# Kernel tuning notes

Measured on AMD Instinct MI355X. Metric: run time of the kernel, lower is better.

The kernel has to match this reference:

```python
import jax, jax.numpy as jnp
import numpy as np

BN_EPS = 1e-5
L2_EPS = 1e-12


def setup_inputs() -> dict:
    key = jax.random.key(0)
    ks = jax.random.split(key, 4)
    B, C, H, W = 16, 384, 56, 56
    x = jax.random.normal(ks[0], (B, C, H, W), dtype=jnp.float32)
    w_qkv = jax.random.normal(ks[1], (3 * C, C), dtype=jnp.float32) * (1.0 / np.sqrt(C))
    b_qkv = jnp.zeros((3 * C,), dtype=jnp.float32)
    w_proj = jax.random.normal(ks[2], (C, C), dtype=jnp.float32) * (1.0 / np.sqrt(C))
    b_proj = jnp.zeros((C,), dtype=jnp.float32)
    bn_gamma = jnp.ones((C,), dtype=jnp.float32)
    bn_beta = jnp.zeros((C,), dtype=jnp.float32)
    bn_mean = jnp.zeros((C,), dtype=jnp.float32)
    bn_var = jnp.ones((C,), dtype=jnp.float32)
    temperature = jnp.ones((1,), dtype=jnp.float32)
    return {"x": x, "w_qkv": w_qkv, "b_qkv": b_qkv, "w_proj": w_proj,
            "b_proj": b_proj, "bn_gamma": bn_gamma, "bn_beta": bn_beta,
            "bn_mean": bn_mean, "bn_var": bn_var, "temperature": temperature}


def _l2norm_lastdim(t):
    # F.normalize(t, dim=-1): divide by max(||t||_2, eps)
    n = jnp.sqrt(jnp.sum(t * t, axis=-1, keepdims=True))
    return t / jnp.maximum(n, L2_EPS)


def reference(x, w_qkv, b_qkv, w_proj, b_proj, bn_gamma, bn_beta, bn_mean, bn_var, temperature):
    B, C, H, W = x.shape
    N = H * W
    # BatchNorm2d (eval mode, running stats)
    scale = bn_gamma / jnp.sqrt(bn_var + BN_EPS)          # [C]
    shift = bn_beta - bn_mean * scale                     # [C]
    xn = x * scale[None, :, None, None] + shift[None, :, None, None]
    # 1x1 conv qkv: C -> 3C, operate on flattened spatial [B, C, N]
    xn_f = xn.reshape(B, C, N)
    qkv = jnp.einsum('oc,bcn->bon', w_qkv, xn_f) + b_qkv[None, :, None]  # [B,3C,N]
    q, k, v = qkv[:, :C], qkv[:, C:2 * C], qkv[:, 2 * C:]
    q = _l2norm_lastdim(q)                                # [B,C,N]
    k = _l2norm_lastdim(k)
    # channel-transposed attention: [B,C,C]
    logits = jnp.einsum('bcn,bdn->bcd', q, k) * temperature[0]
    attn = jax.nn.softmax(logits, axis=-1)
    fused = jnp.einsum('bcd,bdn->bcn', attn, v)           # [B,C,N]
    # 1x1 proj conv + residual
    out = jnp.einsum('oc,bcn->bon', w_proj, fused) + b_proj[None, :, None]
    return x + out.reshape(B, C, H, W)
```

## Files before the change

### kernel.cpp

```cpp
#include <hip/hip_runtime.h>

#define BATCH 16
#define CCH   384
#define NSP   3136
#define NSPP  3200
#define OQKV  1152
#define KSPL  5

typedef unsigned short u16;
typedef float  f32x4  __attribute__((ext_vector_type(4)));
typedef __bf16 bf16x8 __attribute__((ext_vector_type(8)));

__device__ __forceinline__ float bf2f(u16 u) {
  union { unsigned int i; float f; } v; v.i = ((unsigned int)u) << 16; return v.f;
}
__device__ __forceinline__ u16 f2bf(float f) {
  union { float f; unsigned int i; } v; v.f = f;
  unsigned int i = v.i;
  return (u16)((i + 0x7fffu + ((i >> 16) & 1u)) >> 16);
}
__device__ __forceinline__ float rdf(const void* p, long i, bool bf) {
  return bf ? bf2f(((const u16*)p)[i]) : ((const float*)p)[i];
}

__device__ __forceinline__ void gload_lds16(const u16* g, u16* l) {
  __builtin_amdgcn_global_load_lds(
      (const __attribute__((address_space(1))) void*)g,
      (__attribute__((address_space(3))) void*)l, 16, 0, 0);
}

__global__ void transpose_kernel(const void* __restrict__ x, u16* __restrict__ xt,
                                 const u16* __restrict__ probe) {
  const bool bf = (probe[0] == 0x3F80u);
  __shared__ float Ls[32 * 65];
  const int t = threadIdx.x;
  const int n0 = blockIdx.x * 64, c0 = blockIdx.y * 32, b = blockIdx.z;
  if (n0 >= NSP) {
    const int n_l = t >> 2, c8 = (t & 3) * 8;
    uint4 zq = make_uint4(0, 0, 0, 0);
    *(uint4*)(xt + ((long)b * NSPP + n0 + n_l) * CCH + c0 + c8) = zq;
    return;
  }
  {
    const int c_l = t >> 3, n8 = (t & 7) * 8;
    const long src = ((long)b * CCH + c0 + c_l) * NSP + n0 + n8;
    float v[8];
    if (bf) {
      union { uint4 q; u16 e[8]; } u; u.q = *(const uint4*)((const u16*)x + src);
      #pragma unroll
      for (int i = 0; i < 8; i++) v[i] = bf2f(u.e[i]);
    } else {
      float4 a = *(const float4*)((const float*)x + src);
      float4 c = *(const float4*)((const float*)x + src + 4);
      v[0]=a.x; v[1]=a.y; v[2]=a.z; v[3]=a.w; v[4]=c.x; v[5]=c.y; v[6]=c.z; v[7]=c.w;
    }
    #pragma unroll
    for (int i = 0; i < 8; i++) Ls[c_l * 65 + n8 + i] = v[i];
  }
  __syncthreads();
  {
    const int n_l = t >> 2, c8 = (t & 3) * 8;
    union { uint4 q; u16 e[8]; } o;
    #pragma unroll
    for (int i = 0; i < 8; i++) o.e[i] = f2bf(Ls[(c8 + i) * 65 + n_l]);
    *(uint4*)(xt + ((long)b * NSPP + n0 + n_l) * CCH + c0 + c8) = o.q;
  }
}

__global__ void prep_kernel(const void* __restrict__ w_qkv, const void* __restrict__ b_qkv,
                            const void* __restrict__ gamma, const void* __restrict__ beta,
                            const void* __restrict__ mean,  const void* __restrict__ var,
                            const void* __restrict__ b_proj, const void* __restrict__ w_proj,
                            u16* __restrict__ w_eff, float* __restrict__ b_eff,
                            float* __restrict__ bproj_f, u16* __restrict__ wp_bf,
                            const u16* __restrict__ probe) {
  const bool bf = (probe[0] == 0x3F80u);
  __shared__ float s_scale[CCH], s_shift[CCH];
  const int tid = threadIdx.x;
  for (int c = tid; c < CCH; c += 128) {
    float g = rdf(gamma, c, bf), bt = rdf(beta, c, bf);
    float mn = rdf(mean, c, bf), vr = rdf(var, c, bf);
    float sc = g * rsqrtf(vr + 1e-5f);
    s_scale[c] = sc; s_shift[c] = bt - mn * sc;
  }
  __syncthreads();
  const int o = blockIdx.x;
  float part = 0.f;
  for (int c = tid; c < CCH; c += 128) {
    float w = rdf(w_qkv, (long)o * CCH + c, bf);
    w_eff[o * CCH + c] = f2bf(w * s_scale[c]);
    part += w * s_shift[c];
  }
  for (int off = 32; off > 0; off >>= 1) part += __shfl_down(part, off, 64);
  __shared__ float s_part[2];
  if ((tid & 63) == 0) s_part[tid >> 6] = part;
  __syncthreads();
  if (tid == 0) b_eff[o] = rdf(b_qkv, o, bf) + s_part[0] + s_part[1];
  if (o < CCH) {
    for (int c = tid; c < CCH; c += 128)
      wp_bf[o * CCH + c] = f2bf(rdf(w_proj, (long)o * CCH + c, bf));
  }
  if (o == 0) {
    for (int c = tid; c < CCH; c += 128) bproj_f[c] = rdf(b_proj, c, bf);
  }
}

__global__ void zero_kernel(float4* __restrict__ p, long n4) {
  for (long i = (long)blockIdx.x * blockDim.x + threadIdx.x; i < n4;
       i += (long)gridDim.x * blockDim.x)
    p[i] = make_float4(0.f, 0.f, 0.f, 0.f);
}

template<int BM, int BN, int WGM, int WGN, int OUTM, bool BIASM, bool BIASN, bool RES,
         int KS, bool QKN, int NCHK>
__launch_bounds__(256)
__global__ void gemm_nt(const u16* __restrict__ A, const u16* __restrict__ B,
                        void* __restrict__ Cv,
                        const float* __restrict__ biasm, const float* __restrict__ biasn,
                        const void* __restrict__ resv,
                        int K, int lda, int ldb, int ldc,
                        long sA, long sB, long sC, long sRes, int zb, int nLim,
                        float* __restrict__ qns,
                        const u16* __restrict__ probe) {
  constexpr int WM = BM / WGM, WN = BN / WGN;
  constexpr int FM = WM / 16,  FN = WN / 16;
  constexpr int NA = BM / 32,  NB = BN / 32;
  const bool f32io = (probe[0] != 0x3F80u);
  __shared__ __align__(16) u16 As[BM * 64];
  __shared__ __align__(16) u16 Bs[BN * 64];
  const int tid = threadIdx.x, wave = tid >> 6, lane = tid & 63;
  const int quad = lane >> 4, l16 = lane & 15;
  const int wm = wave / WGN, wn = wave % WGN;
  int z = blockIdx.z, kc = 0;
  if (KS > 1) { kc = z % KS; z /= KS; }
  A += z * sA; B += z * sB;
  const long cOff = (long)(zb + z) * sC;
  const long rOff = (long)(zb + z) * sRes;

  const int gx = gridDim.x;
  const int tot = gx * gridDim.y;
  const int wg = blockIdx.y * gx + blockIdx.x;
  const int qq = tot >> 3, rr = tot & 7;
  const int xcd = wg & 7, idx = wg >> 3;
  const int nid = (xcd < rr ? xcd * (qq + 1) : rr * (qq + 1) + (xcd - rr) * qq) + idx;
  const int m0 = (nid % gx) * BM, n0 = (nid / gx) * BN;

  const int kLen = K / KS, kBeg = kc * kLen;

  const u16* ag[NA];
  const u16* bg[NB];
  #pragma unroll
  for (int p = 0; p < NA; p++) {
    int u = tid + p * 256, r = u >> 3, k8 = u & 7;
    ag[p] = A + (long)(m0 + r) * lda + kBeg + ((k8 ^ (r & 7)) << 3);
  }
  #pragma unroll
  for (int p = 0; p < NB; p++) {
    int u = tid + p * 256, r = u >> 3, k8 = u & 7;
    bg[p] = B + (long)(n0 + r) * ldb + kBeg + ((k8 ^ (r & 7)) << 3);
  }

  f32x4 acc[FM][FN] = {};

  const int nt = kLen >> 6;
  for (int t = 0; t < nt; t++) {
    #pragma unroll
    for (int p = 0; p < NA; p++) { gload_lds16(ag[p], &As[(p * 256 + wave * 64) * 8]); ag[p] += 64; }
    #pragma unroll
    for (int p = 0; p < NB; p++) { gload_lds16(bg[p], &Bs[(p * 256 + wave * 64) * 8]); bg[p] += 64; }
    __syncthreads();

    #pragma unroll
    for (int tt = 0; tt < 2; tt++) {
      bf16x8 af[FM], bfr[FN];
      #pragma unroll
      for (int f = 0; f < FM; f++) {
        int r = wm * WM + f * 16 + l16;
        af[f] = *(const bf16x8*)&As[r * 64 + (((tt * 4 + quad) ^ (l16 & 7)) << 3)];
      }
      #pragma unroll
      for (int g = 0; g < FN; g++) {
        int r = wn * WN + g * 16 + l16;
        bfr[g] = *(const bf16x8*)&Bs[r * 64 + (((tt * 4 + quad) ^ (l16 & 7)) << 3)];
      }
      #pragma unroll
      for (int f = 0; f < FM; f++)
        #pragma unroll
        for (int g = 0; g < FN; g++)
          acc[f][g] = __builtin_amdgcn_mfma_f32_16x16x32_bf16(af[f], bfr[g], acc[f][g], 0, 0, 0);
    }
    __syncthreads();
  }

  #pragma unroll
  for (int f = 0; f < FM; f++) {
    #pragma unroll
    for (int reg = 0; reg < 4; reg++) {
      const int mm = m0 + wm * WM + f * 16 + quad * 4 + reg;
      float s2 = 0.f;
      #pragma unroll
      for (int g = 0; g < FN; g++) {
        int nn = n0 + wn * WN + g * 16 + l16;
        float v = acc[f][g][reg];
        if (BIASM) v += biasm[mm];
        if (BIASN) v += biasn[nn];
        if (NCHK == 1 && nn >= nLim) v = 0.f;
        long off = (long)mm * ldc + nn;
        bool live = (NCHK != 2) || (nn < nLim);
        if (RES && live) {
          long ro = rOff + off;
          v += f32io ? ((const float*)resv)[ro] : bf2f(((const u16*)resv)[ro]);
        }
        if (OUTM == 1) {
          long po = cOff + off + ((KS > 1) ? (long)kc * sRes : 0L);
          ((float*)Cv)[po] = v;
        } else if (OUTM == 2) {
          if (live) {
            if (f32io) ((float*)Cv)[cOff + off] = v;
            else       ((u16*)Cv)[cOff + off]   = f2bf(v);
          }
        } else {
          ((u16*)Cv)[cOff + off] = f2bf(v);
        }
        if (QKN) s2 += v * v;
      }
      if (QKN) {
        s2 += __shfl_xor(s2, 1, 16);
        s2 += __shfl_xor(s2, 2, 16);
        s2 += __shfl_xor(s2, 4, 16);
        s2 += __shfl_xor(s2, 8, 16);
        if (l16 == 0) atomicAdd(qns + (long)(zb + z) * 768 + mm, s2);
      }
    }
  }
}

__global__ void softmax_kernel(const float* __restrict__ logits, const float* __restrict__ sums,
                               const void* __restrict__ temp, u16* __restrict__ attn,
                               int zb, const u16* __restrict__ probe) {
  const bool bfm = (probe[0] == 0x3F80u);
  const int c = blockIdx.x, b = blockIdx.y;
  const long base = ((long)b * KSPL) * (CCH * CCH) + (long)c * CCH;
  const float rq = 1.f / fmaxf(sqrtf(sums[(zb + b) * 768 + c]), 1e-12f);
  const float T = rdf(temp, 0, bfm);
  const int tid = threadIdx.x;
  float v[3]; float mx = -1e30f;
  #pragma unroll
  for (int j = 0; j < 3; j++) {
    int d = tid + j * 128;
    float lv = 0.f;
    #pragma unroll
    for (int kc = 0; kc < KSPL; kc++) lv += logits[base + (long)kc * CCH * CCH + d];
    float rd = 1.f / fmaxf(sqrtf(sums[(zb + b) * 768 + 384 + d]), 1e-12f);
    float xv = lv * rq * rd * T;
    v[j] = xv; mx = fmaxf(mx, xv);
  }
  for (int off = 32; off > 0; off >>= 1) mx = fmaxf(mx, __shfl_down(mx, off, 64));
  __shared__ float sm[2];
  if ((tid & 63) == 0) sm[tid >> 6] = mx;
  __syncthreads();
  mx = fmaxf(sm[0], sm[1]);
  float s = 0.f;
  #pragma unroll
  for (int j = 0; j < 3; j++) { v[j] = __expf(v[j] - mx); s += v[j]; }
  for (int off = 32; off > 0; off >>= 1) s += __shfl_down(s, off, 64);
  __shared__ float ss[2];
  if ((tid & 63) == 0) ss[tid >> 6] = s;
  __syncthreads();
  s = ss[0] + ss[1];
  const float inv = 1.f / s;
  u16* arow = attn + ((long)b * CCH + c) * CCH;
  #pragma unroll
  for (int j = 0; j < 3; j++) arow[tid + j * 128] = f2bf(v[j] * inv);
}

extern "C" void kernel_launch(void* const* d_in, const int* in_sizes, int n_in,
                              void* d_out, int out_size, void* d_ws, size_t ws_size,
                              hipStream_t stream) {
  const void* x      = d_in[0];
  const void* w_qkv  = d_in[1];
  const void* b_qkv  = d_in[2];
  const void* w_proj = d_in[3];
  const void* b_proj = d_in[4];
  const void* gamma  = d_in[5];
  const void* beta   = d_in[6];
  const void* mean   = d_in[7];
  const void* var    = d_in[8];
  const void* temp   = d_in[9];
  const u16* probe = (const u16*)gamma;

  const size_t SZ_XT    = (size_t)BATCH * NSPP * CCH * 2;
  const size_t SZ_WEFF  = (size_t)OQKV * CCH * 2;
  const size_t SZ_WPBF  = (size_t)CCH * CCH * 2;
  const size_t SZ_BEFF  = (size_t)OQKV * 4;
  const size_t SZ_BPROJ = (size_t)CCH * 4;
  const size_t SZ_SUMS  = (size_t)BATCH * 768 * 4;
  const size_t SZ_QK_B  = (size_t)768 * NSPP * 2;
  const size_t SZ_VT_B  = (size_t)NSPP * CCH * 2;
  const size_t SZ_FT_B  = (size_t)NSPP * CCH * 2;
  const size_t SZ_LOG_B = (size_t)KSPL * CCH * CCH * 4;
  const size_t SZ_ATT_B = (size_t)CCH * CCH * 2;
  const size_t P = SZ_QK_B + SZ_VT_B + SZ_FT_B + SZ_LOG_B + SZ_ATT_B;
  const size_t FIXED = SZ_XT + SZ_WEFF + SZ_WPBF + SZ_BEFF + SZ_BPROJ + SZ_SUMS;

  long chunk = 1;
  if (ws_size >= FIXED + P) {
    chunk = (long)((ws_size - FIXED) / P);
    if (chunk > BATCH) chunk = BATCH;
    if (chunk < 1) chunk = 1;
  }

  char* ws = (char*)d_ws;
  u16*   xt      = (u16*)ws;   ws += SZ_XT;
  u16*   w_eff   = (u16*)ws;   ws += SZ_WEFF;
  u16*   wp_bf   = (u16*)ws;   ws += SZ_WPBF;
  float* b_eff   = (float*)ws; ws += SZ_BEFF;
  float* bproj_f = (float*)ws; ws += SZ_BPROJ;
  float* sums    = (float*)ws; ws += SZ_SUMS;
  float* logits  = (float*)ws; ws += SZ_LOG_B * chunk;
  u16*   attn    = (u16*)ws;   ws += SZ_ATT_B * chunk;
  u16*   qk      = (u16*)ws;   ws += SZ_QK_B * chunk;
  u16*   v_t     = (u16*)ws;   ws += SZ_VT_B * chunk;
  u16*   fused_t = (u16*)ws;   ws += SZ_FT_B * chunk;

  transpose_kernel<<<dim3(NSPP / 64, CCH / 32, BATCH), dim3(256), 0, stream>>>(x, xt, probe);
  prep_kernel<<<dim3(OQKV), dim3(128), 0, stream>>>(
      w_qkv, b_qkv, gamma, beta, mean, var, b_proj, w_proj,
      w_eff, b_eff, bproj_f, wp_bf, probe);
  zero_kernel<<<dim3(12), dim3(256), 0, stream>>>((float4*)sums, (long)BATCH * 768 / 4);

  const long sX  = (long)CCH * NSP;
  const long sXT = (long)NSPP * CCH;
  const long sQK = (long)768 * NSPP;
  const long sVT = (long)NSPP * CCH;
  const long sFT = (long)NSPP * CCH;
  const long sLG = (long)KSPL * CCH * CCH;
  const long sAT = (long)CCH * CCH;

  for (long b0 = 0; b0 < BATCH; b0 += chunk) {
    const int nb = (int)((BATCH - b0) < chunk ? (BATCH - b0) : chunk);
    const u16* xtb = xt + b0 * sXT;

    gemm_nt<128, 128, 2, 2, 0, true, false, false, 1, true, 1>
        <<<dim3(6, 25, nb), dim3(256), 0, stream>>>(
        w_eff, xtb, qk, b_eff, nullptr, nullptr,
        CCH, CCH, CCH, NSPP, 0L, sXT, sQK, 0L, (int)b0, NSP, sums, probe);

    gemm_nt<128, 128, 2, 2, 0, false, true, false, 1, false, 0>
        <<<dim3(25, 3, nb), dim3(256), 0, stream>>>(
        xtb, w_eff + (long)768 * CCH, v_t, nullptr, b_eff + 768, nullptr,
        CCH, CCH, CCH, CCH, sXT, 0L, sVT, 0L, 0, 0, nullptr, probe);

    gemm_nt<128, 128, 2, 2, 1, false, false, false, KSPL, false, 0>
        <<<dim3(3, 3, nb * KSPL), dim3(256), 0, stream>>>(
        qk, qk + (long)CCH * NSPP, logits, nullptr, nullptr, nullptr,
        NSPP, NSPP, NSPP, CCH, sQK, sQK, sLG, (long)CCH * CCH, 0, 0, nullptr, probe);

    softmax_kernel<<<dim3(CCH, nb), dim3(128), 0, stream>>>(
        logits, sums, temp, attn, (int)b0, probe);

    gemm_nt<128, 128, 2, 2, 0, false, false, false, 1, false, 0>
        <<<dim3(25, 3, nb), dim3(256), 0, stream>>>(
        v_t, attn, fused_t, nullptr, nullptr, nullptr,
        CCH, CCH, CCH, CCH, sVT, sAT, sFT, 0L, 0, 0, nullptr, probe);

    gemm_nt<128, 128, 2, 2, 2, true, false, true, 1, false, 2>
        <<<dim3(3, 25, nb), dim3(256), 0, stream>>>(
        wp_bf, fused_t, d_out, bproj_f, nullptr, x,
        CCH, CCH, CCH, NSP, 0L, sFT, sX, sX, (int)b0, NSP, nullptr, probe);
  }
}
```

Before: 439.5 us.

## Double-buffer LDS tiles in gemm_nt to overlap global loads with MFMA

Splits the shared-memory A/B tiles into two buffers and restructures the K loop so the next tile's global_load_lds is issued while MFMAs run on the current one. Partial vmcnt waits and explicit barriers replace the full sync after each tile, so global-load latency is meant to be hidden behind compute. The cost is twice the LDS per block, which may lower occupancy. The hardcoded vmcnt(8) assumes exactly eight loads per stage (NA+NB==8), so any template instantiation with a different count could wait on the wrong loads.

```diff
diff --git a/kernel.cpp b/kernel.cpp
--- a/kernel.cpp
+++ b/kernel.cpp
@@ -10,6 +10,9 @@
 typedef unsigned short u16;
 typedef float  f32x4  __attribute__((ext_vector_type(4)));
 typedef __bf16 bf16x8 __attribute__((ext_vector_type(8)));
+
+#define WAITV(N) asm volatile("s_waitcnt vmcnt(%0)" :: "n"(N) : "memory")
+#define BARR do { __builtin_amdgcn_s_barrier(); __builtin_amdgcn_sched_barrier(0); } while (0)
 
 __device__ __forceinline__ float bf2f(u16 u) {
   union { unsigned int i; float f; } v; v.i = ((unsigned int)u) << 16; return v.f;
@@ -126,8 +129,10 @@
   constexpr int FM = WM / 16,  FN = WN / 16;
   constexpr int NA = BM / 32,  NB = BN / 32;
   const bool f32io = (probe[0] != 0x3F80u);
-  __shared__ __align__(16) u16 As[BM * 64];
-  __shared__ __align__(16) u16 Bs[BN * 64];
+  __shared__ __align__(16) u16 As0[BM * 64];
+  __shared__ __align__(16) u16 As1[BM * 64];
+  __shared__ __align__(16) u16 Bs0[BN * 64];
+  __shared__ __align__(16) u16 Bs1[BN * 64];
   const int tid = threadIdx.x, wave = tid >> 6, lane = tid & 63;
   const int quad = lane >> 4, l16 = lane & 15;
   const int wm = wave / WGN, wn = wave % WGN;
@@ -162,26 +167,25 @@
 
   f32x4 acc[FM][FN] = {};
 
-  const int nt = kLen >> 6;
-  for (int t = 0; t < nt; t++) {
-    #pragma unroll
-    for (int p = 0; p < NA; p++) { gload_lds16(ag[p], &As[(p * 256 + wave * 64) * 8]); ag[p] += 64; }
-    #pragma unroll
-    for (int p = 0; p < NB; p++) { gload_lds16(bg[p], &Bs[(p * 256 + wave * 64) * 8]); bg[p] += 64; }
-    __syncthreads();
-
+  auto stage = [&](u16* dA, u16* dB) {
+    #pragma unroll
+    for (int p = 0; p < NA; p++) { gload_lds16(ag[p], dA + (p * 256 + wave * 64) * 8); ag[p] += 64; }
+    #pragma unroll
+    for (int p = 0; p < NB; p++) { gload_lds16(bg[p], dB + (p * 256 + wave * 64) * 8); bg[p] += 64; }
+  };
+  auto compute = [&](const u16* sAp, const u16* sBp) {
     #pragma unroll
     for (int tt = 0; tt < 2; tt++) {
       bf16x8 af[FM], bfr[FN];
       #pragma unroll
       for (int f = 0; f < FM; f++) {
         int r = wm * WM + f * 16 + l16;
-        af[f] = *(const bf16x8*)&As[r * 64 + (((tt * 4 + quad) ^ (l16 & 7)) << 3)];
+        af[f] = *(const bf16x8*)&sAp[r * 64 + (((tt * 4 + quad) ^ (l16 & 7)) << 3)];
       }
       #pragma unroll
       for (int g = 0; g < FN; g++) {
         int r = wn * WN + g * 16 + l16;
-        bfr[g] = *(const bf16x8*)&Bs[r * 64 + (((tt * 4 + quad) ^ (l16 & 7)) << 3)];
+        bfr[g] = *(const bf16x8*)&sBp[r * 64 + (((tt * 4 + quad) ^ (l16 & 7)) << 3)];
       }
       #pragma unroll
       for (int f = 0; f < FM; f++)
@@ -189,7 +193,27 @@
         for (int g = 0; g < FN; g++)
           acc[f][g] = __builtin_amdgcn_mfma_f32_16x16x32_bf16(af[f], bfr[g], acc[f][g], 0, 0, 0);
     }
-    __syncthreads();
+  };
+
+  const int nt = kLen >> 6;
+  stage(As0, Bs0);
+  if (nt > 1) { stage(As1, Bs1); WAITV(8); }
+  else        { WAITV(0); }
+  BARR;
+  int t = 0;
+  while (true) {
+    compute(As0, Bs0);
+    if (++t == nt) break;
+    BARR;
+    if (t + 1 < nt) { stage(As0, Bs0); WAITV(8); }
+    else            { WAITV(0); }
+    BARR;
+    compute(As1, Bs1);
+    if (++t == nt) break;
+    BARR;
+    if (t + 1 < nt) { stage(As1, Bs1); WAITV(8); }
+    else            { WAITV(0); }
+    BARR;
   }
 
   #pragma unroll
```

New measurement: 468.3 us. +6.6%, slower.

## Reformulate attention via Gram matrix of input instead of materializing QKV

Applied to the files above, without the earlier changes.

The QKV projection over all spatial positions is replaced by a per-batch Gram matrix G = X·Xᵀ (symmetric, only lower blocks computed, split-K with a reduce kernel). Logits, the q/k norms and the bias corrections then come from small CxC products with the weights (Wq·G·Wkᵀ plus rank-one terms from row sums of X). The value and output projections are folded into one CxC matrix Wp·Wv·attn that is applied to X in a single final GEMM. This removes the large Q/K/V and fused intermediates and most of the spatial-dimension GEMM work, but adds many small kernels and uses hi/lo bf16 splitting to limit precision loss in the reassociated products.

```diff
diff --git a/kernel.cpp b/kernel.cpp
--- a/kernel.cpp
+++ b/kernel.cpp
@@ -4,8 +4,6 @@
 #define CCH   384
 #define NSP   3136
 #define NSPP  3200
-#define OQKV  1152
-#define KSPL  5
 
 typedef unsigned short u16;
 typedef float  f32x4  __attribute__((ext_vector_type(4)));
@@ -30,7 +28,7 @@
 }
 
 __global__ void transpose_kernel(const void* __restrict__ x, u16* __restrict__ xt,
-                                 const u16* __restrict__ probe) {
+                                 u16* __restrict__ xbf, const u16* __restrict__ probe) {
   const bool bf = (probe[0] == 0x3F80u);
   __shared__ float Ls[32 * 65];
   const int t = threadIdx.x;
@@ -54,8 +52,10 @@
       float4 c = *(const float4*)((const float*)x + src + 4);
       v[0]=a.x; v[1]=a.y; v[2]=a.z; v[3]=a.w; v[4]=c.x; v[5]=c.y; v[6]=c.z; v[7]=c.w;
     }
-    #pragma unroll
-    for (int i = 0; i < 8; i++) Ls[c_l * 65 + n8 + i] = v[i];
+    union { uint4 q; u16 e[8]; } ob;
+    #pragma unroll
+    for (int i = 0; i < 8; i++) { ob.e[i] = f2bf(v[i]); Ls[c_l * 65 + n8 + i] = v[i]; }
+    *(uint4*)(xbf + src) = ob.q;
   }
   __syncthreads();
   {
@@ -72,7 +72,9 @@
                             const void* __restrict__ mean,  const void* __restrict__ var,
                             const void* __restrict__ b_proj, const void* __restrict__ w_proj,
                             u16* __restrict__ w_eff, float* __restrict__ b_eff,
-                            float* __restrict__ bproj_f, u16* __restrict__ wp_bf,
+                            float* __restrict__ bproj_f,
+                            unsigned* __restrict__ w2qk, unsigned* __restrict__ wp2,
+                            u16* __restrict__ wvT,
                             const u16* __restrict__ probe) {
   const bool bf = (probe[0] == 0x3F80u);
   __shared__ float s_scale[CCH], s_shift[CCH];
@@ -88,7 +90,10 @@
   float part = 0.f;
   for (int c = tid; c < CCH; c += 128) {
     float w = rdf(w_qkv, (long)o * CCH + c, bf);
-    w_eff[o * CCH + c] = f2bf(w * s_scale[c]);
+    u16 wv = f2bf(w * s_scale[c]);
+    w_eff[(long)o * CCH + c] = wv;
+    if (o < 768) w2qk[(long)o * CCH + c] = (unsigned)wv | ((unsigned)wv << 16);
+    else         wvT[(long)c * CCH + (o - 768)] = wv;
     part += w * s_shift[c];
   }
   for (int off = 32; off > 0; off >>= 1) part += __shfl_down(part, off, 64);
@@ -97,8 +102,10 @@
   __syncthreads();
   if (tid == 0) b_eff[o] = rdf(b_qkv, o, bf) + s_part[0] + s_part[1];
   if (o < CCH) {
-    for (int c = tid; c < CCH; c += 128)
-      wp_bf[o * CCH + c] = f2bf(rdf(w_proj, (long)o * CCH + c, bf));
+    for (int c = tid; c < CCH; c += 128) {
+      u16 pv = f2bf(rdf(w_proj, (long)o * CCH + c, bf));
+      wp2[(long)o * CCH + c] = (unsigned)pv | ((unsigned)pv << 16);
+    }
   }
   if (o == 0) {
     for (int c = tid; c < CCH; c += 128) bproj_f[c] = rdf(b_proj, c, bf);
@@ -111,16 +118,18 @@
     p[i] = make_float4(0.f, 0.f, 0.f, 0.f);
 }
 
-template<int BM, int BN, int WGM, int WGN, int OUTM, bool BIASM, bool BIASN, bool RES,
-         int KS, bool QKN, int NCHK>
+template<int BM, int BN, int WGM, int WGN, int OUTM, bool BIASM, bool RES,
+         int NCHK, bool EPIL, bool SUMX, bool SYMM>
 __launch_bounds__(256)
 __global__ void gemm_nt(const u16* __restrict__ A, const u16* __restrict__ B,
                         void* __restrict__ Cv,
-                        const float* __restrict__ biasm, const float* __restrict__ biasn,
+                        const float* __restrict__ biasm,
                         const void* __restrict__ resv,
                         int K, int lda, int ldb, int ldc,
-                        long sA, long sB, long sC, long sRes, int zb, int nLim,
-                        float* __restrict__ qns,
+                        long sA, long sB, long sC, long sRes,
+                        int zb, int nLim, int ks, int sBM,
+                        float* __restrict__ qns, const u16* __restrict__ epW,
+                        float* __restrict__ sxp,
                         const u16* __restrict__ probe) {
   constexpr int WM = BM / WGM, WN = BN / WGN;
   constexpr int FM = WM / 16,  FN = WN / 16;
@@ -132,7 +141,7 @@
   const int quad = lane >> 4, l16 = lane & 15;
   const int wm = wave / WGN, wn = wave % WGN;
   int z = blockIdx.z, kc = 0;
-  if (KS > 1) { kc = z % KS; z /= KS; }
+  if (ks > 1) { kc = z % ks; z /= ks; }
   A += z * sA; B += z * sB;
   const long cOff = (long)(zb + z) * sC;
   const long rOff = (long)(zb + z) * sRes;
@@ -144,8 +153,9 @@
   const int xcd = wg & 7, idx = wg >> 3;
   const int nid = (xcd < rr ? xcd * (qq + 1) : rr * (qq + 1) + (xcd - rr) * qq) + idx;
   const int m0 = (nid % gx) * BM, n0 = (nid / gx) * BN;
-
-  const int kLen = K / KS, kBeg = kc * kLen;
+  if (SYMM && n0 > m0) return;
+
+  const int kLen = K / ks, kBeg = kc * kLen;
 
   const u16* ag[NA];
   const u16* bg[NB];
@@ -161,6 +171,7 @@
   }
 
   f32x4 acc[FM][FN] = {};
+  float rs[FM] = {};
 
   const int nt = kLen >> 6;
   for (int t = 0; t < nt; t++) {
@@ -182,6 +193,14 @@
       for (int g = 0; g < FN; g++) {
         int r = wn * WN + g * 16 + l16;
         bfr[g] = *(const bf16x8*)&Bs[r * 64 + (((tt * 4 + quad) ^ (l16 & 7)) << 3)];
+      }
+      if (SUMX) {
+        if (n0 == 0 && wn == 0) {
+          #pragma unroll
+          for (int f = 0; f < FM; f++)
+            #pragma unroll
+            for (int j = 0; j < 8; j++) rs[f] += (float)af[f][j];
+        }
       }
       #pragma unroll
       for (int f = 0; f < FM; f++)
@@ -192,6 +211,18 @@
     __syncthreads();
   }
 
+  if (SUMX) {
+    if (n0 == 0 && wn == 0) {
+      #pragma unroll
+      for (int f = 0; f < FM; f++) {
+        float r = rs[f];
+        r += __shfl_xor(r, 16, 64);
+        r += __shfl_xor(r, 32, 64);
+        if (quad == 0) atomicAdd(sxp + (long)z * CCH + m0 + wm * WM + f * 16 + l16, r);
+      }
+    }
+  }
+
   #pragma unroll
   for (int f = 0; f < FM; f++) {
     #pragma unroll
@@ -202,29 +233,34 @@
       for (int g = 0; g < FN; g++) {
         int nn = n0 + wn * WN + g * 16 + l16;
         float v = acc[f][g][reg];
-        if (BIASM) v += biasm[mm];
-        if (BIASN) v += biasn[nn];
-        if (NCHK == 1 && nn >= nLim) v = 0.f;
+        if (BIASM) v += biasm[(long)(zb + z) * sBM + mm];
         long off = (long)mm * ldc + nn;
-        bool live = (NCHK != 2) || (nn < nLim);
+        bool live = true;
+        if (NCHK == 2) live = (nn < nLim);
+        if (NCHK == 3) live = (mm < nLim);
         if (RES && live) {
           long ro = rOff + off;
           v += f32io ? ((const float*)resv)[ro] : bf2f(((const u16*)resv)[ro]);
         }
+        if (EPIL) s2 += v * bf2f(epW[(long)mm * CCH + nn]);
         if (OUTM == 1) {
-          long po = cOff + off + ((KS > 1) ? (long)kc * sRes : 0L);
-          ((float*)Cv)[po] = v;
+          ((float*)Cv)[cOff + off + (long)kc * sRes] = v;
         } else if (OUTM == 2) {
           if (live) {
             if (f32io) ((float*)Cv)[cOff + off] = v;
             else       ((u16*)Cv)[cOff + off]   = f2bf(v);
           }
+        } else if (OUTM == 4) {
+          if (live) {
+            u16 hi = f2bf(v);
+            u16 lo = f2bf(v - bf2f(hi));
+            ((unsigned*)Cv)[cOff + off] = (unsigned)hi | ((unsigned)lo << 16);
+          }
         } else {
-          ((u16*)Cv)[cOff + off] = f2bf(v);
+          if (live) ((u16*)Cv)[cOff + off] = f2bf(v);
         }
-        if (QKN) s2 += v * v;
-      }
-      if (QKN) {
+      }
+      if (EPIL) {
         s2 += __shfl_xor(s2, 1, 16);
         s2 += __shfl_xor(s2, 2, 16);
         s2 += __shfl_xor(s2, 4, 16);
@@ -235,25 +271,61 @@
   }
 }
 
-__global__ void softmax_kernel(const float* __restrict__ logits, const float* __restrict__ sums,
-                               const void* __restrict__ temp, u16* __restrict__ attn,
-                               int zb, const u16* __restrict__ probe) {
+__global__ void greduce_kernel(const float* __restrict__ Gp, unsigned* __restrict__ Gs,
+                               int kspl) {
+  const int b = blockIdx.y;
+  const int idx = blockIdx.x * 256 + threadIdx.x;
+  const int r = idx / CCH, c = idx % CCH;
+  const long e = ((r >> 7) >= (c >> 7)) ? ((long)r * CCH + c) : ((long)c * CCH + r);
+  const long base = (long)b * kspl * (CCH * CCH);
+  float s = 0.f;
+  for (int k = 0; k < kspl; k++) s += Gp[base + (long)k * (CCH * CCH) + e];
+  u16 hi = f2bf(s);
+  u16 lo = f2bf(s - bf2f(hi));
+  Gs[(long)b * (CCH * CCH) + idx] = (unsigned)hi | ((unsigned)lo << 16);
+}
+
+__global__ void ugemv_kernel(const u16* __restrict__ w_eff, const float* __restrict__ sx,
+                             float* __restrict__ u) {
+  const int m = blockIdx.x, b = blockIdx.y, l = threadIdx.x;
+  float s = 0.f;
+  for (int k = l; k < CCH; k += 64) s += bf2f(w_eff[(long)m * CCH + k]) * sx[b * CCH + k];
+  for (int off = 32; off > 0; off >>= 1) s += __shfl_down(s, off, 64);
+  if (l == 0) u[b * 768 + m] = s;
+}
+
+__global__ void cgemv_kernel(const unsigned* __restrict__ wp2, const float* __restrict__ av,
+                             const float* __restrict__ bproj, float* __restrict__ cvec) {
+  const int o = blockIdx.x, b = blockIdx.y, l = threadIdx.x;
+  float s = 0.f;
+  for (int c = l; c < CCH; c += 64)
+    s += bf2f((u16)(wp2[(long)o * CCH + c] & 0xffffu)) * av[b * CCH + c];
+  for (int off = 32; off > 0; off >>= 1) s += __shfl_down(s, off, 64);
+  if (l == 0) cvec[b * CCH + o] = s + bproj[o];
+}
+
+__global__ void softmax_kernel(const float* __restrict__ Lg, const float* __restrict__ qn2,
+                               const float* __restrict__ u, const float* __restrict__ beff,
+                               const void* __restrict__ temp,
+                               u16* __restrict__ attn, float* __restrict__ av,
+                               const u16* __restrict__ probe) {
   const bool bfm = (probe[0] == 0x3F80u);
-  const int c = blockIdx.x, b = blockIdx.y;
-  const long base = ((long)b * KSPL) * (CCH * CCH) + (long)c * CCH;
-  const float rq = 1.f / fmaxf(sqrtf(sums[(zb + b) * 768 + c]), 1e-12f);
+  const int c = blockIdx.x, b = blockIdx.y, tid = threadIdx.x;
+  const float* row = Lg + ((long)b * CCH + c) * CCH;
+  const float beq = beff[c], uq = u[b * 768 + c];
+  const float qn = qn2[b * 768 + c] + 2.f * beq * uq + 3136.f * beq * beq;
+  const float rq = 1.f / fmaxf(sqrtf(fmaxf(qn, 0.f)), 1e-12f);
   const float T = rdf(temp, 0, bfm);
-  const int tid = threadIdx.x;
   float v[3]; float mx = -1e30f;
   #pragma unroll
   for (int j = 0; j < 3; j++) {
     int d = tid + j * 128;
-    float lv = 0.f;
-    #pragma unroll
-    for (int kc = 0; kc < KSPL; kc++) lv += logits[base + (long)kc * CCH * CCH + d];
-    float rd = 1.f / fmaxf(sqrtf(sums[(zb + b) * 768 + 384 + d]), 1e-12f);
-    float xv = lv * rq * rd * T;
-    v[j] = xv; mx = fmaxf(mx, xv);
+    float bek = beff[384 + d], uk = u[b * 768 + 384 + d];
+    float kn = qn2[b * 768 + 384 + d] + 2.f * bek * uk + 3136.f * bek * bek;
+    float rd = 1.f / fmaxf(sqrtf(fmaxf(kn, 0.f)), 1e-12f);
+    float lg = row[d] + uq * bek + beq * uk + 3136.f * beq * bek;
+    v[j] = lg * rq * rd * T;
+    mx = fmaxf(mx, v[j]);
   }
   for (int off = 32; off > 0; off >>= 1) mx = fmaxf(mx, __shfl_down(mx, off, 64));
   __shared__ float sm[2];
@@ -269,9 +341,19 @@
   __syncthreads();
   s = ss[0] + ss[1];
   const float inv = 1.f / s;
+  float avp = 0.f;
   u16* arow = attn + ((long)b * CCH + c) * CCH;
   #pragma unroll
-  for (int j = 0; j < 3; j++) arow[tid + j * 128] = f2bf(v[j] * inv);
+  for (int j = 0; j < 3; j++) {
+    float p = v[j] * inv;
+    arow[tid + j * 128] = f2bf(p);
+    avp += p * beff[768 + tid + j * 128];
+  }
+  for (int off = 32; off > 0; off >>= 1) avp += __shfl_down(avp, off, 64);
+  __shared__ float sa[2];
+  if ((tid & 63) == 0) sa[tid >> 6] = avp;
+  __syncthreads();
+  if (tid == 0) av[b * CCH + c] = sa[0] + sa[1];
 }
 
 extern "C" void kernel_launch(void* const* d_in, const int* in_sizes, int n_in,
@@ -289,84 +371,101 @@
   const void* temp   = d_in[9];
   const u16* probe = (const u16*)gamma;
 
-  const size_t SZ_XT    = (size_t)BATCH * NSPP * CCH * 2;
-  const size_t SZ_WEFF  = (size_t)OQKV * CCH * 2;
-  const size_t SZ_WPBF  = (size_t)CCH * CCH * 2;
-  const size_t SZ_BEFF  = (size_t)OQKV * 4;
-  const size_t SZ_BPROJ = (size_t)CCH * 4;
-  const size_t SZ_SUMS  = (size_t)BATCH * 768 * 4;
-  const size_t SZ_QK_B  = (size_t)768 * NSPP * 2;
-  const size_t SZ_VT_B  = (size_t)NSPP * CCH * 2;
-  const size_t SZ_FT_B  = (size_t)NSPP * CCH * 2;
-  const size_t SZ_LOG_B = (size_t)KSPL * CCH * CCH * 4;
-  const size_t SZ_ATT_B = (size_t)CCH * CCH * 2;
-  const size_t P = SZ_QK_B + SZ_VT_B + SZ_FT_B + SZ_LOG_B + SZ_ATT_B;
-  const size_t FIXED = SZ_XT + SZ_WEFF + SZ_WPBF + SZ_BEFF + SZ_BPROJ + SZ_SUMS;
-
-  long chunk = 1;
-  if (ws_size >= FIXED + P) {
-    chunk = (long)((ws_size - FIXED) / P);
-    if (chunk > BATCH) chunk = BATCH;
-    if (chunk < 1) chunk = 1;
-  }
+  const size_t SZ_XT   = (size_t)BATCH * NSPP * CCH * 2;
+  const size_t SZ_XBF  = (size_t)BATCH * CCH * NSP * 2;
+  const size_t SZ_WEFF = (size_t)1152 * CCH * 2;
+  const size_t SZ_W2QK = (size_t)768 * CCH * 4;
+  const size_t SZ_WP2  = (size_t)CCH * CCH * 4;
+  const size_t SZ_WVT  = (size_t)CCH * CCH * 2;
+  const size_t SZ_BEFF = (size_t)1152 * 4;
+  const size_t SZ_BPRJ = (size_t)CCH * 4;
+  const size_t SZ_SUMS = (size_t)BATCH * (CCH + 768) * 4;
+  const size_t SZ_U    = (size_t)BATCH * 768 * 4;
+  const size_t SZ_AV   = (size_t)BATCH * CCH * 4;
+  const size_t SZ_CV   = (size_t)BATCH * CCH * 4;
+  const size_t SZ_MM   = (size_t)BATCH * CCH * CCH;
+  const size_t FIXED = SZ_XT + SZ_XBF + SZ_WEFF + SZ_W2QK + SZ_WP2 + SZ_WVT +
+                       SZ_BEFF + SZ_BPRJ + SZ_SUMS + SZ_U + SZ_AV + SZ_CV +
+                       SZ_MM * 4  + SZ_MM * 4  + SZ_MM * 4  +
+                       SZ_MM * 2  + SZ_MM * 4  + SZ_MM * 2 ;
+  int kspl = 7;
+  if (ws_size < FIXED + (size_t)BATCH * 7 * CCH * CCH * 4) kspl = 1;
 
   char* ws = (char*)d_ws;
-  u16*   xt      = (u16*)ws;   ws += SZ_XT;
-  u16*   w_eff   = (u16*)ws;   ws += SZ_WEFF;
-  u16*   wp_bf   = (u16*)ws;   ws += SZ_WPBF;
-  float* b_eff   = (float*)ws; ws += SZ_BEFF;
-  float* bproj_f = (float*)ws; ws += SZ_BPROJ;
-  float* sums    = (float*)ws; ws += SZ_SUMS;
-  float* logits  = (float*)ws; ws += SZ_LOG_B * chunk;
-  u16*   attn    = (u16*)ws;   ws += SZ_ATT_B * chunk;
-  u16*   qk      = (u16*)ws;   ws += SZ_QK_B * chunk;
-  u16*   v_t     = (u16*)ws;   ws += SZ_VT_B * chunk;
-  u16*   fused_t = (u16*)ws;   ws += SZ_FT_B * chunk;
-
-  transpose_kernel<<<dim3(NSPP / 64, CCH / 32, BATCH), dim3(256), 0, stream>>>(x, xt, probe);
-  prep_kernel<<<dim3(OQKV), dim3(128), 0, stream>>>(
+  u16*      xt    = (u16*)ws;      ws += SZ_XT;
+  u16*      xbf   = (u16*)ws;      ws += SZ_XBF;
+  u16*      w_eff = (u16*)ws;      ws += SZ_WEFF;
+  unsigned* w2qk  = (unsigned*)ws; ws += SZ_W2QK;
+  unsigned* wp2   = (unsigned*)ws; ws += SZ_WP2;
+  u16*      wvT   = (u16*)ws;      ws += SZ_WVT;
+  float*    b_eff = (float*)ws;    ws += SZ_BEFF;
+  float*    bproj = (float*)ws;    ws += SZ_BPRJ;
+  float*    sx    = (float*)ws;    ws += (size_t)BATCH * CCH * 4;
+  float*    qn2   = (float*)ws;    ws += (size_t)BATCH * 768 * 4;
+  float*    u     = (float*)ws;    ws += SZ_U;
+  float*    av    = (float*)ws;    ws += SZ_AV;
+  float*    cvec  = (float*)ws;    ws += SZ_CV;
+  unsigned* Gs    = (unsigned*)ws; ws += SZ_MM * 4;
+  unsigned* Ts    = (unsigned*)ws; ws += SZ_MM * 4;
+  float*    Lg    = (float*)ws;    ws += SZ_MM * 4;
+  u16*      attn  = (u16*)ws;      ws += SZ_MM * 2;
+  unsigned* RTs   = (unsigned*)ws; ws += SZ_MM * 4;
+  u16*      Mb    = (u16*)ws;      ws += SZ_MM * 2;
+  float*    Gp    = (float*)ws;
+
+  const long sXB = (long)CCH * NSP;
+  const long sMM = (long)CCH * CCH;
+  const long sM2 = (long)CCH * 768;
+
+  transpose_kernel<<<dim3(NSPP / 64, CCH / 32, BATCH), dim3(256), 0, stream>>>(
+      x, xt, xbf, probe);
+  prep_kernel<<<dim3(1152), dim3(128), 0, stream>>>(
       w_qkv, b_qkv, gamma, beta, mean, var, b_proj, w_proj,
-      w_eff, b_eff, bproj_f, wp_bf, probe);
-  zero_kernel<<<dim3(12), dim3(256), 0, stream>>>((float4*)sums, (long)BATCH * 768 / 4);
-
-  const long sX  = (long)CCH * NSP;
-  const long sXT = (long)NSPP * CCH;
-  const long sQK = (long)768 * NSPP;
-  const long sVT = (long)NSPP * CCH;
-  const long sFT = (long)NSPP * CCH;
-  const long sLG = (long)KSPL * CCH * CCH;
-  const long sAT = (long)CCH * CCH;
-
-  for (long b0 = 0; b0 < BATCH; b0 += chunk) {
-    const int nb = (int)((BATCH - b0) < chunk ? (BATCH - b0) : chunk);
-    const u16* xtb = xt + b0 * sXT;
-
-    gemm_nt<128, 128, 2, 2, 0, true, false, false, 1, true, 1>
-        <<<dim3(6, 25, nb), dim3(256), 0, stream>>>(
-        w_eff, xtb, qk, b_eff, nullptr, nullptr,
-        CCH, CCH, CCH, NSPP, 0L, sXT, sQK, 0L, (int)b0, NSP, sums, probe);
-
-    gemm_nt<128, 128, 2, 2, 0, false, true, false, 1, false, 0>
-        <<<dim3(25, 3, nb), dim3(256), 0, stream>>>(
-        xtb, w_eff + (long)768 * CCH, v_t, nullptr, b_eff + 768, nullptr,
-        CCH, CCH, CCH, CCH, sXT, 0L, sVT, 0L, 0, 0, nullptr, probe);
-
-    gemm_nt<128, 128, 2, 2, 1, false, false, false, KSPL, false, 0>
-        <<<dim3(3, 3, nb * KSPL), dim3(256), 0, stream>>>(
-        qk, qk + (long)CCH * NSPP, logits, nullptr, nullptr, nullptr,
-        NSPP, NSPP, NSPP, CCH, sQK, sQK, sLG, (long)CCH * CCH, 0, 0, nullptr, probe);
-
-    softmax_kernel<<<dim3(CCH, nb), dim3(128), 0, stream>>>(
-        logits, sums, temp, attn, (int)b0, probe);
-
-    gemm_nt<128, 128, 2, 2, 0, false, false, false, 1, false, 0>
-        <<<dim3(25, 3, nb), dim3(256), 0, stream>>>(
-        v_t, attn, fused_t, nullptr, nullptr, nullptr,
-        CCH, CCH, CCH, CCH, sVT, sAT, sFT, 0L, 0, 0, nullptr, probe);
-
-    gemm_nt<128, 128, 2, 2, 2, true, false, true, 1, false, 2>
-        <<<dim3(3, 25, nb), dim3(256), 0, stream>>>(
-        wp_bf, fused_t, d_out, bproj_f, nullptr, x,
-        CCH, CCH, CCH, NSP, 0L, sFT, sX, sX, (int)b0, NSP, nullptr, probe);
-  }
-}
+      w_eff, b_eff, bproj, w2qk, wp2, wvT, probe);
+  zero_kernel<<<dim3(18), dim3(256), 0, stream>>>(
+      (float4*)sx, (long)BATCH * (CCH + 768) / 4);
+
+  gemm_nt<128, 128, 2, 2, 1, false, false, 0, false, true, true>
+      <<<dim3(3, 3, BATCH * kspl), dim3(256), 0, stream>>>(
+      xbf, xbf, Gp, nullptr, nullptr,
+      NSP, NSP, NSP, CCH, sXB, sXB, (long)kspl * sMM, sMM,
+      0, 0, kspl, 0, nullptr, nullptr, sx, probe);
+
+  greduce_kernel<<<dim3(576, BATCH), dim3(256), 0, stream>>>(Gp, Gs, kspl);
+  ugemv_kernel<<<dim3(768, BATCH), dim3(64), 0, stream>>>(w_eff, sx, u);
+
+  gemm_nt<96, 96, 2, 2, 4, false, false, 3, true, false, false>
+      <<<dim3(8, 4, BATCH), dim3(256), 0, stream>>>(
+      (const u16*)w2qk, (const u16*)Gs, Ts, nullptr, nullptr,
+      768, 768, 768, CCH, 0L, sM2, sMM, 0L,
+      0, CCH, 1, 0, qn2, w_eff, nullptr, probe);
+
+  gemm_nt<96, 96, 2, 2, 1, false, false, 0, false, false, false>
+      <<<dim3(4, 4, BATCH), dim3(256), 0, stream>>>(
+      (const u16*)Ts, (const u16*)w2qk + (long)384 * 768, Lg, nullptr, nullptr,
+      768, 768, 768, CCH, sM2, 0L, sMM, 0L,
+      0, 0, 1, 0, nullptr, nullptr, nullptr, probe);
+
+  softmax_kernel<<<dim3(CCH, BATCH), dim3(128), 0, stream>>>(
+      Lg, qn2, u, b_eff, temp, attn, av, probe);
+
+  gemm_nt<96, 96, 2, 2, 4, false, false, 0, false, false, false>
+      <<<dim3(4, 4, BATCH), dim3(256), 0, stream>>>(
+      wvT, attn, RTs, nullptr, nullptr,
+      CCH, CCH, CCH, CCH, 0L, sMM, sMM, 0L,
+      0, 0, 1, 0, nullptr, nullptr, nullptr, probe);
+
+  cgemv_kernel<<<dim3(CCH, BATCH), dim3(64), 0, stream>>>(wp2, av, bproj, cvec);
+
+  gemm_nt<96, 96, 2, 2, 0, false, false, 0, false, false, false>
+      <<<dim3(4, 4, BATCH), dim3(256), 0, stream>>>(
+      (const u16*)wp2, (const u16*)RTs, Mb, nullptr, nullptr,
+      768, 768, 768, CCH, 0L, sM2, sMM, 0L,
+      0, 0, 1, 0, nullptr, nullptr, nullptr, probe);
+
+  gemm_nt<128, 128, 2, 2, 2, true, true, 2, false, false, false>
+      <<<dim3(3, 25, BATCH), dim3(256), 0, stream>>>(
+      Mb, xt, d_out, cvec, x,
+      CCH, CCH, CCH, NSP, sMM, (long)NSPP * CCH, (long)CCH * NSP, (long)CCH * NSP,
+      0, NSP, 1, CCH, nullptr, nullptr, nullptr, probe);
+}
```

Result: faster. 403.0 us (-8.3%).
